# Optimization experiments

Hardware: AMD Instinct MI355X
Metric: run time of the kernel (lower is better)

The kernel has to match this reference:

```python
import jax, jax.numpy as jnp
import numpy as np

B, C, H, W = 16, 256, 128, 128  # H must equal W for this module's dilation trick to be consistent
K = 2  # kernel_size (lifting taps)


def setup_inputs() -> dict:
    key = jax.random.key(0)
    ks = jax.random.split(key, 6)
    C4 = C // 4
    return {
        "x": jax.random.normal(ks[0], (B, C, H, W), jnp.float32),
        "conv1x1_w": jax.random.normal(ks[1], (C, C), jnp.float32) / np.sqrt(C).astype(np.float32),
        "lp_v": jax.random.uniform(ks[2], (C4, 1, K, 1), jnp.float32),  # low_pass_filter_v
        "hp_v": jax.random.uniform(ks[3], (C4, 1, K, 1), jnp.float32),  # high_pass_filter_v
        "lp_h": jax.random.uniform(ks[4], (C4, 1, 1, K), jnp.float32),  # low_pass_filter_h
        "hp_h": jax.random.uniform(ks[5], (C4, 1, 1, K), jnp.float32),  # high_pass_filter_h
    }


def _interleave(e, o, axis):
    # interleave e/o along `axis`: out[..., 2i, ...] = e[..., i, ...], out[..., 2i+1, ...] = o[..., i, ...]
    s = jnp.stack([e, o], axis=axis + 1)
    sh = list(e.shape)
    sh[axis] *= 2
    return s.reshape(sh)


def reference(x, conv1x1_w, lp_v, hp_v, lp_h, hp_h):
    # 1x1 conv (no bias)
    x = jnp.einsum('bchw,oc->bohw', x, conv1x1_w)
    b_, c_, h_, w_ = x.shape
    # pad_mode == 'discard': crop to multiple of kernel_size
    x = x[:, :, :h_ - h_ % K, :w_ - w_ % K]
    c4 = c_ // 4
    a = x[:, :c4]
    bq = x[:, c4:2 * c4]
    cq = x[:, 2 * c4:3 * c4]
    dq = x[:, 3 * c4:]
    # per-channel 2-tap combos: w0 * first_half + w1 * second_half
    lv0 = lp_v[:, 0, 0, 0][None, :, None, None]; lv1 = lp_v[:, 0, 1, 0][None, :, None, None]
    hv0 = hp_v[:, 0, 0, 0][None, :, None, None]; hv1 = hp_v[:, 0, 1, 0][None, :, None, None]
    lh0 = lp_h[:, 0, 0, 0][None, :, None, None]; lh1 = lp_h[:, 0, 0, 1][None, :, None, None]
    hh0 = hp_h[:, 0, 0, 0][None, :, None, None]; hh1 = hp_h[:, 0, 0, 1][None, :, None, None]
    # vertical lifting + row interleave -> [B, C/4, 2H, W]
    x_l = _interleave(lv0 * a + lv1 * bq, hv0 * a + hv1 * bq, 2)
    x_h = _interleave(lv0 * cq + lv1 * dq, hv0 * cq + hv1 * dq, 2)
    # horizontal lifting (valid because H == W) + column interleave -> [B, C/4, 2H, 2W]
    x_e = lh0 * x_l + lh1 * x_h
    x_o = hh0 * x_l + hh1 * x_h
    return _interleave(x_e, x_o, 3)
```

## Files before the change

### kernel.cpp

```cpp
#include <hip/hip_runtime.h>

#define HW 16384
#define LDS_W 72

typedef __attribute__((ext_vector_type(8))) __bf16 bf16x8;
typedef __attribute__((ext_vector_type(4))) float floatx4;
typedef __attribute__((ext_vector_type(4))) unsigned short ushort4_t;
typedef __attribute__((ext_vector_type(8))) unsigned short ushort8_t;

__device__ __forceinline__ unsigned short f2bf(float f) {
    unsigned int u = __builtin_bit_cast(unsigned int, f);
    unsigned int r = (u + 0x7FFFu + ((u >> 16) & 1u)) >> 16;
    return (unsigned short)r;
}

__global__ void wconv_kernel(const float* __restrict__ w, unsigned short* __restrict__ wb) {
    int i = blockIdx.x * 256 + threadIdx.x;
    wb[i] = f2bf(w[i]);
}

__global__ void fused_gemm_lift(const float* __restrict__ x,
                                const unsigned short* __restrict__ wb,
                                const float* __restrict__ lp_v,
                                const float* __restrict__ hp_v,
                                const float* __restrict__ lp_h,
                                const float* __restrict__ hp_h,
                                float* __restrict__ out) {
    __shared__ unsigned short ws_s[256 * LDS_W];
    __shared__ unsigned short xs_s[64 * LDS_W];

    const int tid  = threadIdx.x;
    const int wv   = tid >> 6;
    const int lane = tid & 63;
    const int tile = blockIdx.x & 255;
    const int bb   = blockIdx.x >> 8;
    const int p0   = tile * 64;

    const float* xb = x + (size_t)bb * 256 * HW;

    floatx4 acc[4][4];
    #pragma unroll
    for (int g = 0; g < 4; ++g)
        #pragma unroll
        for (int n = 0; n < 4; ++n) {
            floatx4 z = {0.f, 0.f, 0.f, 0.f};
            acc[g][n] = z;
        }

    const int sp  = tid & 63;
    const int scg = tid >> 6;

    for (int kt = 0; kt < 4; ++kt) {
        const int c0 = kt * 64;
        if (kt) __syncthreads();

        #pragma unroll
        for (int i = 0; i < 8; ++i) {
            int idx  = i * 256 + tid;
            int o    = idx >> 3;
            int koff = (idx & 7) * 8;
            ushort8_t v = *reinterpret_cast<const ushort8_t*>(wb + o * 256 + c0 + koff);
            *reinterpret_cast<ushort8_t*>(&ws_s[o * LDS_W + koff]) = v;
        }

        {
            const float* xsrc = xb + (size_t)(c0 + scg * 16) * HW + p0 + sp;
            #pragma unroll
            for (int j = 0; j < 4; ++j) {
                ushort4_t v;
                #pragma unroll
                for (int e = 0; e < 4; ++e)
                    v[e] = f2bf(xsrc[(size_t)(j * 4 + e) * HW]);
                *reinterpret_cast<ushort4_t*>(&xs_s[sp * LDS_W + scg * 16 + j * 4]) = v;
            }
        }
        __syncthreads();

        const int lrow = lane & 15;
        const int lk   = (lane >> 4) * 8;
        #pragma unroll
        for (int kc = 0; kc < 2; ++kc) {
            bf16x8 af[4], bfr[4];
            #pragma unroll
            for (int g = 0; g < 4; ++g)
                af[g] = *reinterpret_cast<const bf16x8*>(
                    &ws_s[(g * 64 + wv * 16 + lrow) * LDS_W + kc * 32 + lk]);
            #pragma unroll
            for (int n = 0; n < 4; ++n)
                bfr[n] = *reinterpret_cast<const bf16x8*>(
                    &xs_s[(n * 16 + lrow) * LDS_W + kc * 32 + lk]);
            #pragma unroll
            for (int g = 0; g < 4; ++g)
                #pragma unroll
                for (int n = 0; n < 4; ++n)
                    acc[g][n] = __builtin_amdgcn_mfma_f32_16x16x32_bf16(af[g], bfr[n], acc[g][n], 0, 0, 0);
        }
    }

    const int lrow = lane & 15;
    const int lgr  = lane >> 4;
    #pragma unroll
    for (int ri = 0; ri < 4; ++ri) {
        const int q = wv * 16 + lgr * 4 + ri;
        const float lv0 = lp_v[2 * q], lv1 = lp_v[2 * q + 1];
        const float hv0 = hp_v[2 * q], hv1 = hp_v[2 * q + 1];
        const float lh0 = lp_h[2 * q], lh1 = lp_h[2 * q + 1];
        const float hh0 = hp_h[2 * q], hh1 = hp_h[2 * q + 1];
        float* outq = out + (size_t)(bb * 64 + q) * 65536;
        #pragma unroll
        for (int n = 0; n < 4; ++n) {
            const int p = p0 + n * 16 + lrow;
            const int h = p >> 7;
            const int w = p & 127;
            const float a  = acc[0][n][ri];
            const float b2 = acc[1][n][ri];
            const float c2 = acc[2][n][ri];
            const float d2 = acc[3][n][ri];
            const float xl0 = lv0 * a + lv1 * b2;
            const float xl1 = hv0 * a + hv1 * b2;
            const float xh0 = lv0 * c2 + lv1 * d2;
            const float xh1 = hv0 * c2 + hv1 * d2;
            float2 r0 = make_float2(lh0 * xl0 + lh1 * xh0, hh0 * xl0 + hh1 * xh0);
            float2 r1 = make_float2(lh0 * xl1 + lh1 * xh1, hh0 * xl1 + hh1 * xh1);
            *reinterpret_cast<float2*>(outq + (size_t)(2 * h) * 256 + 2 * w)     = r0;
            *reinterpret_cast<float2*>(outq + (size_t)(2 * h + 1) * 256 + 2 * w) = r1;
        }
    }
}

extern "C" void kernel_launch(void* const* d_in, const int* in_sizes, int n_in,
                              void* d_out, int out_size, void* d_ws, size_t ws_size,
                              hipStream_t stream) {
    const float* x   = (const float*)d_in[0];
    const float* w   = (const float*)d_in[1];
    const float* lpv = (const float*)d_in[2];
    const float* hpv = (const float*)d_in[3];
    const float* lph = (const float*)d_in[4];
    const float* hph = (const float*)d_in[5];
    float* outp = (float*)d_out;
    unsigned short* wb = (unsigned short*)d_ws;

    wconv_kernel<<<dim3(256), dim3(256), 0, stream>>>(w, wb);
    fused_gemm_lift<<<dim3(4096), dim3(256), 0, stream>>>(x, wb, lpv, hpv, lph, hph, outp);
}
```

Baseline: 132.4 us.

## Read bf16 weights directly from global and split N across 8 waves

The weight tile is no longer staged in LDS; each wave loads its MFMA A-fragments straight from the global bf16 weight buffer, which should hit in L2 and L1. Blocks grow to 512 threads, with the 8 waves split into 4 M-groups times 2 N-halves, so each wave keeps fewer accumulators. The x staging is spread over more threads with one 8-wide LDS store per thread. The aim is to shrink LDS use and register pressure to raise occupancy and latency hiding, at the cost of redundant global weight reads across waves and blocks.

Result: slower. 185.4 us (+40.0%).

```diff
diff --git a/kernel.cpp b/kernel.cpp
--- a/kernel.cpp
+++ b/kernel.cpp
@@ -5,7 +5,6 @@
 
 typedef __attribute__((ext_vector_type(8))) __bf16 bf16x8;
 typedef __attribute__((ext_vector_type(4))) float floatx4;
-typedef __attribute__((ext_vector_type(4))) unsigned short ushort4_t;
 typedef __attribute__((ext_vector_type(8))) unsigned short ushort8_t;
 
 __device__ __forceinline__ unsigned short f2bf(float f) {
@@ -19,30 +18,35 @@
     wb[i] = f2bf(w[i]);
 }
 
-__global__ void fused_gemm_lift(const float* __restrict__ x,
-                                const unsigned short* __restrict__ wb,
-                                const float* __restrict__ lp_v,
-                                const float* __restrict__ hp_v,
-                                const float* __restrict__ lp_h,
-                                const float* __restrict__ hp_h,
-                                float* __restrict__ out) {
-    __shared__ unsigned short ws_s[256 * LDS_W];
+__global__ __launch_bounds__(512, 4) void fused_gemm_lift(
+        const float* __restrict__ x,
+        const unsigned short* __restrict__ wb,
+        const float* __restrict__ lp_v,
+        const float* __restrict__ hp_v,
+        const float* __restrict__ lp_h,
+        const float* __restrict__ hp_h,
+        float* __restrict__ out) {
     __shared__ unsigned short xs_s[64 * LDS_W];
 
-    const int tid  = threadIdx.x;
-    const int wv   = tid >> 6;
-    const int lane = tid & 63;
-    const int tile = blockIdx.x & 255;
-    const int bb   = blockIdx.x >> 8;
-    const int p0   = tile * 64;
+    const int tid   = threadIdx.x;
+    const int wv    = tid >> 6;
+    const int lane  = tid & 63;
+    const int mgrp  = wv & 3;
+    const int nhalf = wv >> 2;
+    const int tile  = blockIdx.x & 255;
+    const int bb    = blockIdx.x >> 8;
+    const int p0    = tile * 64;
 
     const float* xb = x + (size_t)bb * 256 * HW;
 
-    floatx4 acc[4][4];
+    const int lrow = lane & 15;
+    const int lk8  = (lane >> 4) * 8;
+
+    floatx4 acc[4][2];
     #pragma unroll
     for (int g = 0; g < 4; ++g)
         #pragma unroll
-        for (int n = 0; n < 4; ++n) {
+        for (int n = 0; n < 2; ++n) {
             floatx4 z = {0.f, 0.f, 0.f, 0.f};
             acc[g][n] = z;
         }
@@ -54,62 +58,47 @@
         const int c0 = kt * 64;
         if (kt) __syncthreads();
 
-        #pragma unroll
-        for (int i = 0; i < 8; ++i) {
-            int idx  = i * 256 + tid;
-            int o    = idx >> 3;
-            int koff = (idx & 7) * 8;
-            ushort8_t v = *reinterpret_cast<const ushort8_t*>(wb + o * 256 + c0 + koff);
-            *reinterpret_cast<ushort8_t*>(&ws_s[o * LDS_W + koff]) = v;
-        }
-
         {
-            const float* xsrc = xb + (size_t)(c0 + scg * 16) * HW + p0 + sp;
+            const float* xsrc = xb + (size_t)(c0 + scg * 8) * HW + p0 + sp;
+            ushort8_t v;
             #pragma unroll
-            for (int j = 0; j < 4; ++j) {
-                ushort4_t v;
-                #pragma unroll
-                for (int e = 0; e < 4; ++e)
-                    v[e] = f2bf(xsrc[(size_t)(j * 4 + e) * HW]);
-                *reinterpret_cast<ushort4_t*>(&xs_s[sp * LDS_W + scg * 16 + j * 4]) = v;
-            }
+            for (int j = 0; j < 8; ++j)
+                v[j] = f2bf(xsrc[(size_t)j * HW]);
+            *reinterpret_cast<ushort8_t*>(&xs_s[sp * LDS_W + scg * 8]) = v;
         }
         __syncthreads();
 
-        const int lrow = lane & 15;
-        const int lk   = (lane >> 4) * 8;
         #pragma unroll
         for (int kc = 0; kc < 2; ++kc) {
-            bf16x8 af[4], bfr[4];
+            bf16x8 af[4], bfr[2];
             #pragma unroll
             for (int g = 0; g < 4; ++g)
                 af[g] = *reinterpret_cast<const bf16x8*>(
-                    &ws_s[(g * 64 + wv * 16 + lrow) * LDS_W + kc * 32 + lk]);
+                    wb + (size_t)(g * 64 + mgrp * 16 + lrow) * 256 + c0 + kc * 32 + lk8);
             #pragma unroll
-            for (int n = 0; n < 4; ++n)
+            for (int n = 0; n < 2; ++n)
                 bfr[n] = *reinterpret_cast<const bf16x8*>(
-                    &xs_s[(n * 16 + lrow) * LDS_W + kc * 32 + lk]);
+                    &xs_s[((nhalf * 2 + n) * 16 + lrow) * LDS_W + kc * 32 + lk8]);
             #pragma unroll
             for (int g = 0; g < 4; ++g)
                 #pragma unroll
-                for (int n = 0; n < 4; ++n)
+                for (int n = 0; n < 2; ++n)
                     acc[g][n] = __builtin_amdgcn_mfma_f32_16x16x32_bf16(af[g], bfr[n], acc[g][n], 0, 0, 0);
         }
     }
 
-    const int lrow = lane & 15;
-    const int lgr  = lane >> 4;
+    const int lgr = lane >> 4;
     #pragma unroll
     for (int ri = 0; ri < 4; ++ri) {
-        const int q = wv * 16 + lgr * 4 + ri;
+        const int q = mgrp * 16 + lgr * 4 + ri;
         const float lv0 = lp_v[2 * q], lv1 = lp_v[2 * q + 1];
         const float hv0 = hp_v[2 * q], hv1 = hp_v[2 * q + 1];
         const float lh0 = lp_h[2 * q], lh1 = lp_h[2 * q + 1];
         const float hh0 = hp_h[2 * q], hh1 = hp_h[2 * q + 1];
         float* outq = out + (size_t)(bb * 64 + q) * 65536;
         #pragma unroll
-        for (int n = 0; n < 4; ++n) {
-            const int p = p0 + n * 16 + lrow;
+        for (int n = 0; n < 2; ++n) {
+            const int p = p0 + (nhalf * 2 + n) * 16 + lrow;
             const int h = p >> 7;
             const int w = p & 127;
             const float a  = acc[0][n][ri];
@@ -141,5 +130,5 @@
     unsigned short* wb = (unsigned short*)d_ws;
 
     wconv_kernel<<<dim3(256), dim3(256), 0, stream>>>(w, wb);
-    fused_gemm_lift<<<dim3(4096), dim3(256), 0, stream>>>(x, wb, lpv, hpv, lph, hph, outp);
+    fused_gemm_lift<<<dim3(4096), dim3(512), 0, stream>>>(x, wb, lpv, hpv, lph, hph, outp);
 }
```

## Double-buffer weights via direct global-to-LDS loads and prefetch x in registers

Applied to the files above, without the earlier changes.

The weight-conversion kernel now writes bf16 weights pre-tiled per K-chunk with an XOR swizzle, so the GEMM kernel can copy them straight into LDS with global_load_lds into a double buffer. Each block doubles to 512 threads and 128 pixels, and the next chunk of x is prefetched into registers while the MFMAs run on the current chunk. Swizzled LDS indexing replaces row padding to avoid bank conflicts. The aim is to hide global load latency behind compute and cut staging overhead, at the cost of more LDS per block (about 80 KB), extra barriers and higher register pressure.

New measurement: 132.5 us. About the same (+0.1%).

```diff
diff --git a/kernel.cpp b/kernel.cpp
--- a/kernel.cpp
+++ b/kernel.cpp
@@ -1,12 +1,13 @@
 #include <hip/hip_runtime.h>
 
 #define HW 16384
-#define LDS_W 72
 
 typedef __attribute__((ext_vector_type(8))) __bf16 bf16x8;
 typedef __attribute__((ext_vector_type(4))) float floatx4;
-typedef __attribute__((ext_vector_type(4))) unsigned short ushort4_t;
 typedef __attribute__((ext_vector_type(8))) unsigned short ushort8_t;
+
+typedef const __attribute__((address_space(1))) unsigned int gu32;
+typedef __attribute__((address_space(3))) unsigned int lu32;
 
 __device__ __forceinline__ unsigned short f2bf(float f) {
     unsigned int u = __builtin_bit_cast(unsigned int, f);
@@ -14,29 +15,48 @@
     return (unsigned short)r;
 }
 
+__device__ __forceinline__ void gload_lds16(const unsigned short* g, unsigned short* l) {
+    __builtin_amdgcn_global_load_lds((gu32*)g, (lu32*)l, 16, 0, 0);
+}
+
 __global__ void wconv_kernel(const float* __restrict__ w, unsigned short* __restrict__ wb) {
     int i = blockIdx.x * 256 + threadIdx.x;
-    wb[i] = f2bf(w[i]);
+    int row = i >> 8, c = i & 255;
+    int kt = c >> 6, kl = c & 63;
+    int idx = (row * 64 + kl) ^ ((row & 7) << 3);
+    wb[kt * 16384 + idx] = f2bf(w[i]);
 }
 
-__global__ void fused_gemm_lift(const float* __restrict__ x,
-                                const unsigned short* __restrict__ wb,
-                                const float* __restrict__ lp_v,
-                                const float* __restrict__ hp_v,
-                                const float* __restrict__ lp_h,
-                                const float* __restrict__ hp_h,
-                                float* __restrict__ out) {
-    __shared__ unsigned short ws_s[256 * LDS_W];
-    __shared__ unsigned short xs_s[64 * LDS_W];
+__global__ __launch_bounds__(512, 4) void fused_gemm_lift(
+        const float* __restrict__ x,
+        const unsigned short* __restrict__ wb,
+        const float* __restrict__ lp_v,
+        const float* __restrict__ hp_v,
+        const float* __restrict__ lp_h,
+        const float* __restrict__ hp_h,
+        float* __restrict__ out) {
+    __shared__ alignas(16) unsigned short wbuf_s[2][16384];
+    __shared__ alignas(16) unsigned short xbuf_s[8192];
 
     const int tid  = threadIdx.x;
     const int wv   = tid >> 6;
     const int lane = tid & 63;
-    const int tile = blockIdx.x & 255;
-    const int bb   = blockIdx.x >> 8;
-    const int p0   = tile * 64;
+    const int mgrp  = wv & 3;
+    const int nhalf = wv >> 2;
+    const int tile = blockIdx.x & 127;
+    const int bb   = blockIdx.x >> 7;
+    const int p0   = tile * 128;
 
     const float* xb = x + (size_t)bb * 256 * HW;
+
+    const int lrow  = lane & 15;
+    const int khalf = lane >> 4;
+    const int fswz  = (lrow & 7) << 3;
+
+    const int px  = tid & 127;
+    const int cb  = (tid >> 7) * 16;
+    const int xw0 = (px * 64 + cb) ^ ((px & 7) << 3);
+    const int xw1 = (px * 64 + cb + 8) ^ ((px & 7) << 3);
 
     floatx4 acc[4][4];
     #pragma unroll
@@ -47,61 +67,73 @@
             acc[g][n] = z;
         }
 
-    const int sp  = tid & 63;
-    const int scg = tid >> 6;
+    float xv[16];
+
+    {
+        const float* xs = xb + (size_t)cb * HW + p0 + px;
+        #pragma unroll
+        for (int j = 0; j < 16; ++j) xv[j] = xs[(size_t)j * HW];
+        #pragma unroll
+        for (int pass = 0; pass < 4; ++pass) {
+            int ch = pass * 512 + wv * 64;
+            gload_lds16(wb + (size_t)(ch + lane) * 8, &wbuf_s[0][ch * 8]);
+        }
+        ushort8_t v0, v1;
+        #pragma unroll
+        for (int j = 0; j < 8; ++j) { v0[j] = f2bf(xv[j]); v1[j] = f2bf(xv[8 + j]); }
+        *reinterpret_cast<ushort8_t*>(&xbuf_s[xw0]) = v0;
+        *reinterpret_cast<ushort8_t*>(&xbuf_s[xw1]) = v1;
+    }
+    __syncthreads();
 
     for (int kt = 0; kt < 4; ++kt) {
-        const int c0 = kt * 64;
-        if (kt) __syncthreads();
+        const int cw = kt & 1;
 
-        #pragma unroll
-        for (int i = 0; i < 8; ++i) {
-            int idx  = i * 256 + tid;
-            int o    = idx >> 3;
-            int koff = (idx & 7) * 8;
-            ushort8_t v = *reinterpret_cast<const ushort8_t*>(wb + o * 256 + c0 + koff);
-            *reinterpret_cast<ushort8_t*>(&ws_s[o * LDS_W + koff]) = v;
+        if (kt < 3) {
+            const float* xs = xb + (size_t)((kt + 1) * 64 + cb) * HW + p0 + px;
+            #pragma unroll
+            for (int j = 0; j < 16; ++j) xv[j] = xs[(size_t)j * HW];
+            #pragma unroll
+            for (int pass = 0; pass < 4; ++pass) {
+                int ch = pass * 512 + wv * 64;
+                gload_lds16(wb + (size_t)((kt + 1) * 16384) + (size_t)(ch + lane) * 8,
+                            &wbuf_s[cw ^ 1][ch * 8]);
+            }
         }
 
-        {
-            const float* xsrc = xb + (size_t)(c0 + scg * 16) * HW + p0 + sp;
-            #pragma unroll
-            for (int j = 0; j < 4; ++j) {
-                ushort4_t v;
-                #pragma unroll
-                for (int e = 0; e < 4; ++e)
-                    v[e] = f2bf(xsrc[(size_t)(j * 4 + e) * HW]);
-                *reinterpret_cast<ushort4_t*>(&xs_s[sp * LDS_W + scg * 16 + j * 4]) = v;
-            }
-        }
-        __syncthreads();
-
-        const int lrow = lane & 15;
-        const int lk   = (lane >> 4) * 8;
         #pragma unroll
         for (int kc = 0; kc < 2; ++kc) {
             bf16x8 af[4], bfr[4];
             #pragma unroll
             for (int g = 0; g < 4; ++g)
                 af[g] = *reinterpret_cast<const bf16x8*>(
-                    &ws_s[(g * 64 + wv * 16 + lrow) * LDS_W + kc * 32 + lk]);
+                    &wbuf_s[cw][((g * 64 + mgrp * 16 + lrow) * 64 + kc * 32 + khalf * 8) ^ fswz]);
             #pragma unroll
             for (int n = 0; n < 4; ++n)
                 bfr[n] = *reinterpret_cast<const bf16x8*>(
-                    &xs_s[(n * 16 + lrow) * LDS_W + kc * 32 + lk]);
+                    &xbuf_s[((nhalf * 64 + n * 16 + lrow) * 64 + kc * 32 + khalf * 8) ^ fswz]);
             #pragma unroll
             for (int g = 0; g < 4; ++g)
                 #pragma unroll
                 for (int n = 0; n < 4; ++n)
                     acc[g][n] = __builtin_amdgcn_mfma_f32_16x16x32_bf16(af[g], bfr[n], acc[g][n], 0, 0, 0);
         }
+
+        if (kt < 3) {
+            __syncthreads();
+            ushort8_t v0, v1;
+            #pragma unroll
+            for (int j = 0; j < 8; ++j) { v0[j] = f2bf(xv[j]); v1[j] = f2bf(xv[8 + j]); }
+            *reinterpret_cast<ushort8_t*>(&xbuf_s[xw0]) = v0;
+            *reinterpret_cast<ushort8_t*>(&xbuf_s[xw1]) = v1;
+            __syncthreads();
+        }
     }
 
-    const int lrow = lane & 15;
-    const int lgr  = lane >> 4;
+    const int lgr = lane >> 4;
     #pragma unroll
     for (int ri = 0; ri < 4; ++ri) {
-        const int q = wv * 16 + lgr * 4 + ri;
+        const int q = mgrp * 16 + lgr * 4 + ri;
         const float lv0 = lp_v[2 * q], lv1 = lp_v[2 * q + 1];
         const float hv0 = hp_v[2 * q], hv1 = hp_v[2 * q + 1];
         const float lh0 = lp_h[2 * q], lh1 = lp_h[2 * q + 1];
@@ -109,7 +141,7 @@
         float* outq = out + (size_t)(bb * 64 + q) * 65536;
         #pragma unroll
         for (int n = 0; n < 4; ++n) {
-            const int p = p0 + n * 16 + lrow;
+            const int p = p0 + nhalf * 64 + n * 16 + lrow;
             const int h = p >> 7;
             const int w = p & 127;
             const float a  = acc[0][n][ri];
@@ -138,8 +170,8 @@
     const float* lph = (const float*)d_in[4];
     const float* hph = (const float*)d_in[5];
     float* outp = (float*)d_out;
-    unsigned short* wb = (unsigned short*)d_ws;
+    unsigned short* wbp = (unsigned short*)d_ws;
 
-    wconv_kernel<<<dim3(256), dim3(256), 0, stream>>>(w, wb);
-    fused_gemm_lift<<<dim3(4096), dim3(256), 0, stream>>>(x, wb, lpv, hpv, lph, hph, outp);
+    wconv_kernel<<<dim3(256), dim3(256), 0, stream>>>(w, wbp);
+    fused_gemm_lift<<<dim3(2048), dim3(512), 0, stream>>>(x, wbp, lpv, hpv, lph, hph, outp);
 }
```
